# Performance work log

Measured on AMD Instinct MI355X. Metric: run time of the kernel, lower is better.

The kernel has to match this reference:

```python
import jax, jax.numpy as jnp
import numpy as np

DIM = 128      # size_in
SIGN = 4       # number of leading outputs negated
CONST = 0.618  # additive constant in Linear_v5
BATCH = 4096


def setup_inputs() -> dict:
    key = jax.random.key(0)
    k0, k1, k2, k3, k4 = jax.random.split(key, 5)
    s1 = 1.0 / np.sqrt(DIM)
    s2 = 1.0 / np.sqrt(2 * DIM)
    return {
        "t": 0,
        "input_": jax.random.normal(k0, (BATCH, 2 * DIM), dtype=jnp.float32),
        "W1": jax.random.uniform(k1, (2 * DIM, DIM), jnp.float32, -s1, s1),
        "b1": jax.random.uniform(k2, (2 * DIM,), jnp.float32, -s1, s1),
        "W2": jax.random.uniform(k3, (DIM, 2 * DIM), jnp.float32, -s2, s2),
        "b2": jax.random.uniform(k4, (DIM,), jnp.float32, -s2, s2),
    }


def reference(t, input_, W1, b1, W2, b2):
    x = input_[:, :DIM]   # [B, D]
    v = input_[:, DIM:]   # [B, D]
    dtype = x.dtype
    # sign vector: first SIGN outputs of g are negated (applied after sigmoid+const)
    sgn = jnp.where(jnp.arange(DIM) < SIGN, -1.0, 1.0).astype(dtype)  # [D]

    h = x @ W1.T + b1                      # [B, 2D]
    a = jax.nn.relu(h)
    s = jax.nn.sigmoid(a @ W2.T + b2)      # [B, D]
    g = sgn * (s + CONST)                  # [B, D]

    # Analytic batch Jacobian J[b,i,j] = d g_i / d x_j
    # = sgn_i * s_i(1-s_i) * sum_k W2[i,k] * 1[h_bk>0] * W1[k,j]
    mask = (h > 0).astype(dtype)           # [B, 2D]
    Jcore = jnp.einsum('ik,bk,kj->bij', W2, mask, W1)   # [B, D, D]
    J = (sgn * (s * (1.0 - s)))[:, :, None] * Jcore      # [B, D, D]

    g_inv = 1.0 / g                        # [B, D]
    conn1 = -J * g_inv[:, None, :]         # [B, i, j] * g_inv_j
    conn2 = J * g_inv[:, :, None]          # [B, i, j] * g_inv_i

    dv_vec = v[:, :, None] * v[:, None, :]               # [B, i, j] = v_i v_j
    vtemp1 = jnp.sum((v * v)[:, :, None] * conn1, axis=1)  # sum_i v_i^2 conn1[b,i,j]
    vtemp2 = jnp.einsum('bji,bji->bj', dv_vec, conn2)
    vtemp3 = jnp.einsum('bij,bji->bj', dv_vec, conn2)
    dv = vtemp1 + vtemp2 + vtemp3          # [B, D]

    return jnp.concatenate([v, dv], axis=1)  # [B, 2D]
```

## Files before the change

kernel.cpp:

```cpp
#include <hip/hip_runtime.h>
#include <math.h>

#define DIM    128
#define DIM2   256
#define NSIGN  4
#define CCONST 0.618f
#define MB     16
#define NTHR   512

typedef short bf16x8 __attribute__((ext_vector_type(8)));
typedef float f32x4  __attribute__((ext_vector_type(4)));

#define MFMA(a,b,c) __builtin_amdgcn_mfma_f32_16x16x32_bf16((a),(b),(c),0,0,0)

union BU { uint4 q; bf16x8 b; };

__device__ __forceinline__ unsigned short f2bf(float f) {
    unsigned u = __float_as_uint(f);
    u += 0x7fffu + ((u >> 16) & 1u);
    return (unsigned short)(u >> 16);
}
__device__ __forceinline__ float bf2f(unsigned short h) {
    return __uint_as_float(((unsigned)h) << 16);
}
__device__ __forceinline__ bf16x8 frag16(const unsigned short* p) {
    BU u; u.q = *(const uint4*)p; return u.b;
}

__global__ void prep_pack(const float* __restrict__ W1, const float* __restrict__ W2,
                          unsigned short* __restrict__ pk) {
    int tid  = blockIdx.x * 256 + threadIdx.x;
    int lane = tid & 63;
    int rest = tid >> 6;
    int es   = rest & 3;
    int tkt  = (rest >> 2) & 63;
    int m    = rest >> 8;
    int r0   = ((tkt & ((m == 0 || m == 2) ? 3 : 7)) * 32) + ((lane >> 4) << 3) + es * 2;
    int nt   = tkt / ((m == 0 || m == 2) ? 4 : 8);
    int c    = nt * 16 + (lane & 15);

    unsigned short h[2], l[2];
    #pragma unroll
    for (int d = 0; d < 2; ++d) {
        int r = r0 + d;
        float v;
        if      (m == 0) v = W1[c * DIM  + r];
        else if (m == 1) v = W2[c * DIM2 + r];
        else if (m == 2) v = W2[r * DIM2 + c];
        else             v = W1[r * DIM  + c];
        unsigned short hb = f2bf(v);
        h[d] = hb;
        if (m == 0) l[d] = f2bf(v - bf2f(hb));
    }
    size_t base = (size_t)m * 65536 + (size_t)(tkt * 64 + lane) * 8 + es * 2;
    *(unsigned*)(pk + base) = (unsigned)h[0] | ((unsigned)h[1] << 16);
    if (m == 0)
        *(unsigned*)(pk + base + 32768) = (unsigned)l[0] | ((unsigned)l[1] << 16);
}

__global__ __launch_bounds__(NTHR, 1)
void fused_connection(const float* __restrict__ input_,
                      const float* __restrict__ b1,
                      const float* __restrict__ b2,
                      const unsigned short* __restrict__ pk,
                      float* __restrict__ out) {
    __shared__ __align__(16) float          vv [MB][132];
    __shared__ __align__(16) unsigned short xbH[MB][136];
    __shared__ __align__(16) unsigned short xbL[MB][136];
    __shared__ __align__(16) unsigned short vbH[MB][136];
    __shared__ __align__(16) unsigned short aH [MB][264];
    __shared__ __align__(16) unsigned short mwH[MB][264];
    __shared__ __align__(16) unsigned short vcH[MB][136];

    const int t    = threadIdx.x;
    const int lane = t & 63;
    const int w    = t >> 6;
    const int b0   = blockIdx.x * MB;
    const int arow = lane & 15;
    const int kg   = (lane >> 4) << 3;
    const int rbase = (lane >> 4) << 2;

    const int prow = t >> 5;
    const int pc   = (t & 31) * 8;
    const float4* src = (const float4*)(input_ + (size_t)(b0 + prow) * DIM2 + pc);
    const float4 f0 = src[0];
    const float4 f1 = src[1];

    uint4 b1hq[2][4], b1lq[2][4];
    #pragma unroll
    for (int nt2 = 0; nt2 < 2; ++nt2)
        #pragma unroll
        for (int kt = 0; kt < 4; ++kt) {
            const unsigned short* bp = pk + (size_t)((((w * 2 + nt2) * 4 + kt) * 64 + lane) * 8);
            b1hq[nt2][kt] = *(const uint4*)bp;
            b1lq[nt2][kt] = *(const uint4*)(bp + 32768);
        }
    const float b1v0 = b1[(w * 2 + 0) * 16 + arow];
    const float b1v1 = b1[(w * 2 + 1) * 16 + arow];
    const float b2v  = b2[w * 16 + arow];

    {
        float fa[8] = {f0.x, f0.y, f0.z, f0.w, f1.x, f1.y, f1.z, f1.w};
        if (pc < DIM) {
            union { unsigned short u[8]; uint4 q; } H, L;
            #pragma unroll
            for (int e = 0; e < 8; ++e) {
                unsigned short hb = f2bf(fa[e]);
                H.u[e] = hb;
                L.u[e] = f2bf(fa[e] - bf2f(hb));
            }
            *(uint4*)&xbH[prow][pc] = H.q;
            *(uint4*)&xbL[prow][pc] = L.q;
        } else {
            int c = pc - DIM;
            *(float4*)&vv[prow][c]     = f0;
            *(float4*)&vv[prow][c + 4] = f1;
            union { unsigned short u[8]; uint4 q; } H;
            #pragma unroll
            for (int e = 0; e < 8; ++e) H.u[e] = f2bf(fa[e]);
            *(uint4*)&vbH[prow][c] = H.q;
            float4* op = (float4*)(out + (size_t)(b0 + prow) * DIM2 + c);
            op[0] = f0; op[1] = f1;
        }
    }
    __syncthreads();

    uint4 b2q[8];
    {
        const unsigned short* p1 = pk + 65536;
        #pragma unroll
        for (int kt = 0; kt < 8; ++kt)
            b2q[kt] = *(const uint4*)(p1 + (size_t)((w * 8 + kt) * 64 + lane) * 8);

        bf16x8 xH[4], xL[4], vH[4];
        #pragma unroll
        for (int kt = 0; kt < 4; ++kt) {
            int k0 = kt * 32 + kg;
            xH[kt] = frag16(&xbH[arow][k0]);
            xL[kt] = frag16(&xbL[arow][k0]);
            vH[kt] = frag16(&vbH[arow][k0]);
        }
        #pragma unroll
        for (int nt2 = 0; nt2 < 2; ++nt2) {
            int nt = w * 2 + nt2;
            f32x4 ha = {0.f, 0.f, 0.f, 0.f};
            f32x4 wa = {0.f, 0.f, 0.f, 0.f};
            #pragma unroll
            for (int kt = 0; kt < 4; ++kt) {
                BU bh, bl;
                bh.q = b1hq[nt2][kt];
                bl.q = b1lq[nt2][kt];
                ha = MFMA(xH[kt], bh.b, ha);
                ha = MFMA(xH[kt], bl.b, ha);
                ha = MFMA(xL[kt], bh.b, ha);
                wa = MFMA(vH[kt], bh.b, wa);
            }
            int col  = nt * 16 + arow;
            float bias = nt2 ? b1v1 : b1v0;
            #pragma unroll
            for (int reg = 0; reg < 4; ++reg) {
                int row = rbase + reg;
                float hv = ha[reg] + bias;
                bool  mk = hv > 0.f;
                aH[row][col]  = f2bf(mk ? hv : 0.f);
                mwH[row][col] = f2bf(mk ? wa[reg] : 0.f);
            }
        }
    }
    __syncthreads();

    float sreg[4];
    f32x4 t2a = {0.f, 0.f, 0.f, 0.f};
    uint4 b3q[2][4];
    {
        const unsigned short* p2 = pk + 2 * 65536;
        #pragma unroll
        for (int nt2 = 0; nt2 < 2; ++nt2)
            #pragma unroll
            for (int kt = 0; kt < 4; ++kt)
                b3q[nt2][kt] = *(const uint4*)(p2 + (size_t)((((w * 2 + nt2) * 4 + kt) * 64 + lane) * 8));

        f32x4 za = {0.f, 0.f, 0.f, 0.f};
        #pragma unroll
        for (int kt = 0; kt < 8; ++kt) {
            int k0 = kt * 32 + kg;
            bf16x8 af = frag16(&aH[arow][k0]);
            bf16x8 mf = frag16(&mwH[arow][k0]);
            BU bh; bh.q = b2q[kt];
            za  = MFMA(af, bh.b, za);
            t2a = MFMA(mf, bh.b, t2a);
        }
        int   ci   = w * 16 + arow;
        float sg_i = (ci < NSIGN) ? -1.f : 1.f;
        #pragma unroll
        for (int reg = 0; reg < 4; ++reg) {
            int row = rbase + reg;
            float z = za[reg] + b2v;
            float s = 1.f / (1.f + __expf(-z));
            sreg[reg] = s;
            float vvl = vv[row][ci];
            vcH[row][ci] = f2bf(vvl * vvl * sg_i * s * (1.f - s));
        }
    }
    __syncthreads();

    uint4 b4q[8];
    {
        const unsigned short* p3 = pk + 3 * 65536;
        #pragma unroll
        for (int kt = 0; kt < 8; ++kt)
            b4q[kt] = *(const uint4*)(p3 + (size_t)((w * 8 + kt) * 64 + lane) * 8);

        bf16x8 cH[4];
        #pragma unroll
        for (int kt = 0; kt < 4; ++kt)
            cH[kt] = frag16(&vcH[arow][kt * 32 + kg]);
        #pragma unroll
        for (int nt2 = 0; nt2 < 2; ++nt2) {
            int nt = w * 2 + nt2;
            f32x4 ua = {0.f, 0.f, 0.f, 0.f};
            #pragma unroll
            for (int kt = 0; kt < 4; ++kt) {
                BU bh; bh.q = b3q[nt2][kt];
                ua = MFMA(cH[kt], bh.b, ua);
            }
            int ck = nt * 16 + arow;
            #pragma unroll
            for (int reg = 0; reg < 4; ++reg) {
                int row = rbase + reg;
                bool mk = aH[row][ck] != 0;
                mwH[row][ck] = f2bf(mk ? ua[reg] : 0.f);
            }
        }
    }
    __syncthreads();

    {
        f32x4 t1a = {0.f, 0.f, 0.f, 0.f};
        #pragma unroll
        for (int kt = 0; kt < 8; ++kt) {
            bf16x8 mf = frag16(&mwH[arow][kt * 32 + kg]);
            BU bh; bh.q = b4q[kt];
            t1a = MFMA(mf, bh.b, t1a);
        }
        int   cj   = w * 16 + arow;
        float sg_j = (cj < NSIGN) ? -1.f : 1.f;
        #pragma unroll
        for (int reg = 0; reg < 4; ++reg) {
            int row = rbase + reg;
            float s  = sreg[reg];
            float cv = sg_j * s * (1.f - s);
            float gi = 1.f / (sg_j * (s + CCONST));
            float vvl = vv[row][cj];
            float dv = fmaf(-gi, t1a[reg], 2.f * vvl * gi * cv * t2a[reg]);
            out[(size_t)(b0 + row) * DIM2 + DIM + cj] = dv;
        }
    }
}

extern "C" void kernel_launch(void* const* d_in, const int* in_sizes, int n_in,
                              void* d_out, int out_size, void* d_ws, size_t ws_size,
                              hipStream_t stream) {
    const float* input_ = (const float*)d_in[1];
    const float* W1 = (const float*)d_in[2];
    const float* b1 = (const float*)d_in[3];
    const float* W2 = (const float*)d_in[4];
    const float* b2 = (const float*)d_in[5];
    float* out = (float*)d_out;
    unsigned short* pk = (unsigned short*)d_ws;

    const int batch = in_sizes[1] / DIM2;

    prep_pack<<<256, 256, 0, stream>>>(W1, W2, pk);
    fused_connection<<<batch / MB, NTHR, 0, stream>>>(input_, b1, b2, pk, out);
}
```

Measured before the change: 16.72 us.

## Run each 16-row tile with a single wavefront, replacing barriers with lgkmcnt waits

The block shrinks from eight waves to one. That single wave computes every column tile of all four GEMM stages itself, looping over pairs of N-tiles and loading the packed weights per pair. Because only one wave touches the LDS, the __syncthreads barriers become s_waitcnt lgkmcnt(0), which removes block-level synchronisation. The cost is eight times more serial MFMA work and weight traffic per wave. The launch presumably still uses 256 blocks of one wave each, far fewer waves than the 2048 before, so latency hiding and CU utilisation may suffer.

```diff
diff --git a/kernel.cpp b/kernel.cpp
--- a/kernel.cpp
+++ b/kernel.cpp
@@ -6,14 +6,15 @@
 #define NSIGN  4
 #define CCONST 0.618f
 #define MB     16
-#define NTHR   512
+#define NTHR   64
 
 typedef short bf16x8 __attribute__((ext_vector_type(8)));
 typedef float f32x4  __attribute__((ext_vector_type(4)));
 
 #define MFMA(a,b,c) __builtin_amdgcn_mfma_f32_16x16x32_bf16((a),(b),(c),0,0,0)
-
-union BU { uint4 q; bf16x8 b; };
+#define LGKM0() asm volatile("s_waitcnt lgkmcnt(0)" ::: "memory")
+
+union BU { uint4 q; bf16x8 b; unsigned short u[8]; };
 
 __device__ __forceinline__ unsigned short f2bf(float f) {
     unsigned u = __float_as_uint(f);
@@ -72,188 +73,232 @@
     __shared__ __align__(16) unsigned short mwH[MB][264];
     __shared__ __align__(16) unsigned short vcH[MB][136];
 
-    const int t    = threadIdx.x;
-    const int lane = t & 63;
-    const int w    = t >> 6;
-    const int b0   = blockIdx.x * MB;
-    const int arow = lane & 15;
-    const int kg   = (lane >> 4) << 3;
+    const int lane  = threadIdx.x;
+    const int b0    = blockIdx.x * MB;
+    const int arow  = lane & 15;
+    const int kg    = (lane >> 4) << 3;
     const int rbase = (lane >> 4) << 2;
 
-    const int prow = t >> 5;
-    const int pc   = (t & 31) * 8;
-    const float4* src = (const float4*)(input_ + (size_t)(b0 + prow) * DIM2 + pc);
-    const float4 f0 = src[0];
-    const float4 f1 = src[1];
-
-    uint4 b1hq[2][4], b1lq[2][4];
+    float4 fr[16];
     #pragma unroll
-    for (int nt2 = 0; nt2 < 2; ++nt2)
-        #pragma unroll
-        for (int kt = 0; kt < 4; ++kt) {
-            const unsigned short* bp = pk + (size_t)((((w * 2 + nt2) * 4 + kt) * 64 + lane) * 8);
-            b1hq[nt2][kt] = *(const uint4*)bp;
-            b1lq[nt2][kt] = *(const uint4*)(bp + 32768);
-        }
-    const float b1v0 = b1[(w * 2 + 0) * 16 + arow];
-    const float b1v1 = b1[(w * 2 + 1) * 16 + arow];
-    const float b2v  = b2[w * 16 + arow];
-
-    {
-        float fa[8] = {f0.x, f0.y, f0.z, f0.w, f1.x, f1.y, f1.z, f1.w};
-        if (pc < DIM) {
-            union { unsigned short u[8]; uint4 q; } H, L;
-            #pragma unroll
-            for (int e = 0; e < 8; ++e) {
+    for (int r = 0; r < 16; ++r)
+        fr[r] = *(const float4*)(input_ + (size_t)(b0 + r) * DIM2 + lane * 4);
+
+    if (lane < 32) {
+        const int c = lane * 4;
+        #pragma unroll
+        for (int r = 0; r < 16; ++r) {
+            float fa[4] = {fr[r].x, fr[r].y, fr[r].z, fr[r].w};
+            union { unsigned short u[4]; ushort4 q; } H, L;
+            #pragma unroll
+            for (int e = 0; e < 4; ++e) {
                 unsigned short hb = f2bf(fa[e]);
                 H.u[e] = hb;
                 L.u[e] = f2bf(fa[e] - bf2f(hb));
             }
-            *(uint4*)&xbH[prow][pc] = H.q;
-            *(uint4*)&xbL[prow][pc] = L.q;
-        } else {
-            int c = pc - DIM;
-            *(float4*)&vv[prow][c]     = f0;
-            *(float4*)&vv[prow][c + 4] = f1;
-            union { unsigned short u[8]; uint4 q; } H;
-            #pragma unroll
-            for (int e = 0; e < 8; ++e) H.u[e] = f2bf(fa[e]);
-            *(uint4*)&vbH[prow][c] = H.q;
-            float4* op = (float4*)(out + (size_t)(b0 + prow) * DIM2 + c);
-            op[0] = f0; op[1] = f1;
-        }
-    }
-    __syncthreads();
-
-    uint4 b2q[8];
+            *(ushort4*)&xbH[r][c] = H.q;
+            *(ushort4*)&xbL[r][c] = L.q;
+        }
+    } else {
+        const int c = lane * 4 - DIM;
+        #pragma unroll
+        for (int r = 0; r < 16; ++r) {
+            *(float4*)&vv[r][c] = fr[r];
+            float fa[4] = {fr[r].x, fr[r].y, fr[r].z, fr[r].w};
+            union { unsigned short u[4]; ushort4 q; } H;
+            #pragma unroll
+            for (int e = 0; e < 4; ++e) H.u[e] = f2bf(fa[e]);
+            *(ushort4*)&vbH[r][c] = H.q;
+            *(float4*)(out + (size_t)(b0 + r) * DIM2 + c) = fr[r];
+        }
+    }
+    LGKM0();
+
     {
-        const unsigned short* p1 = pk + 65536;
-        #pragma unroll
-        for (int kt = 0; kt < 8; ++kt)
-            b2q[kt] = *(const uint4*)(p1 + (size_t)((w * 8 + kt) * 64 + lane) * 8);
-
         bf16x8 xH[4], xL[4], vH[4];
         #pragma unroll
         for (int kt = 0; kt < 4; ++kt) {
-            int k0 = kt * 32 + kg;
+            const int k0 = kt * 32 + kg;
             xH[kt] = frag16(&xbH[arow][k0]);
             xL[kt] = frag16(&xbL[arow][k0]);
             vH[kt] = frag16(&vbH[arow][k0]);
         }
         #pragma unroll
-        for (int nt2 = 0; nt2 < 2; ++nt2) {
-            int nt = w * 2 + nt2;
-            f32x4 ha = {0.f, 0.f, 0.f, 0.f};
-            f32x4 wa = {0.f, 0.f, 0.f, 0.f};
+        for (int np = 0; np < 8; ++np) {
+            uint4 bh[2][4], bl[2][4];
+            #pragma unroll
+            for (int j = 0; j < 2; ++j)
+                #pragma unroll
+                for (int kt = 0; kt < 4; ++kt) {
+                    const unsigned short* bp =
+                        pk + (size_t)((((np * 2 + j) * 4 + kt) * 64 + lane) * 8);
+                    bh[j][kt] = *(const uint4*)bp;
+                    bl[j][kt] = *(const uint4*)(bp + 32768);
+                }
+            const float bv0 = b1[(np * 2 + 0) * 16 + arow];
+            const float bv1 = b1[(np * 2 + 1) * 16 + arow];
+            f32x4 ha0 = {0.f,0.f,0.f,0.f}, ha1 = {0.f,0.f,0.f,0.f};
+            f32x4 wa0 = {0.f,0.f,0.f,0.f}, wa1 = {0.f,0.f,0.f,0.f};
             #pragma unroll
             for (int kt = 0; kt < 4; ++kt) {
-                BU bh, bl;
-                bh.q = b1hq[nt2][kt];
-                bl.q = b1lq[nt2][kt];
-                ha = MFMA(xH[kt], bh.b, ha);
-                ha = MFMA(xH[kt], bl.b, ha);
-                ha = MFMA(xL[kt], bh.b, ha);
-                wa = MFMA(vH[kt], bh.b, wa);
-            }
-            int col  = nt * 16 + arow;
-            float bias = nt2 ? b1v1 : b1v0;
-            #pragma unroll
-            for (int reg = 0; reg < 4; ++reg) {
-                int row = rbase + reg;
-                float hv = ha[reg] + bias;
-                bool  mk = hv > 0.f;
-                aH[row][col]  = f2bf(mk ? hv : 0.f);
-                mwH[row][col] = f2bf(mk ? wa[reg] : 0.f);
-            }
-        }
-    }
-    __syncthreads();
-
-    float sreg[4];
-    f32x4 t2a = {0.f, 0.f, 0.f, 0.f};
-    uint4 b3q[2][4];
+                BU h0, l0, h1, l1;
+                h0.q = bh[0][kt]; l0.q = bl[0][kt];
+                h1.q = bh[1][kt]; l1.q = bl[1][kt];
+                ha0 = MFMA(xH[kt], h0.b, ha0);
+                ha1 = MFMA(xH[kt], h1.b, ha1);
+                ha0 = MFMA(xH[kt], l0.b, ha0);
+                ha1 = MFMA(xH[kt], l1.b, ha1);
+                ha0 = MFMA(xL[kt], h0.b, ha0);
+                ha1 = MFMA(xL[kt], h1.b, ha1);
+                wa0 = MFMA(vH[kt], h0.b, wa0);
+                wa1 = MFMA(vH[kt], h1.b, wa1);
+            }
+            #pragma unroll
+            for (int j = 0; j < 2; ++j) {
+                const int   col  = (np * 2 + j) * 16 + arow;
+                const float bias = j ? bv1 : bv0;
+                const f32x4 ha   = j ? ha1 : ha0;
+                const f32x4 wa   = j ? wa1 : wa0;
+                #pragma unroll
+                for (int reg = 0; reg < 4; ++reg) {
+                    const int row = rbase + reg;
+                    float hv = ha[reg] + bias;
+                    bool  mk = hv > 0.f;
+                    aH[row][col]  = f2bf(mk ? hv : 0.f);
+                    mwH[row][col] = f2bf(mk ? wa[reg] : 0.f);
+                }
+            }
+        }
+    }
+    LGKM0();
+
+    float sreg[8][4];
+    f32x4 t2s[8];
     {
-        const unsigned short* p2 = pk + 2 * 65536;
-        #pragma unroll
-        for (int nt2 = 0; nt2 < 2; ++nt2)
-            #pragma unroll
-            for (int kt = 0; kt < 4; ++kt)
-                b3q[nt2][kt] = *(const uint4*)(p2 + (size_t)((((w * 2 + nt2) * 4 + kt) * 64 + lane) * 8));
-
-        f32x4 za = {0.f, 0.f, 0.f, 0.f};
+        bf16x8 af[8], mf[8];
         #pragma unroll
         for (int kt = 0; kt < 8; ++kt) {
-            int k0 = kt * 32 + kg;
-            bf16x8 af = frag16(&aH[arow][k0]);
-            bf16x8 mf = frag16(&mwH[arow][k0]);
-            BU bh; bh.q = b2q[kt];
-            za  = MFMA(af, bh.b, za);
-            t2a = MFMA(mf, bh.b, t2a);
-        }
-        int   ci   = w * 16 + arow;
-        float sg_i = (ci < NSIGN) ? -1.f : 1.f;
-        #pragma unroll
-        for (int reg = 0; reg < 4; ++reg) {
-            int row = rbase + reg;
-            float z = za[reg] + b2v;
-            float s = 1.f / (1.f + __expf(-z));
-            sreg[reg] = s;
-            float vvl = vv[row][ci];
-            vcH[row][ci] = f2bf(vvl * vvl * sg_i * s * (1.f - s));
-        }
-    }
-    __syncthreads();
-
-    uint4 b4q[8];
+            const int k0 = kt * 32 + kg;
+            af[kt] = frag16(&aH[arow][k0]);
+            mf[kt] = frag16(&mwH[arow][k0]);
+        }
+        #pragma unroll
+        for (int cp = 0; cp < 4; ++cp) {
+            uint4 bq[2][8];
+            #pragma unroll
+            for (int j = 0; j < 2; ++j)
+                #pragma unroll
+                for (int kt = 0; kt < 8; ++kt)
+                    bq[j][kt] = *(const uint4*)(pk + 65536 +
+                        (size_t)((((cp * 2 + j) * 8 + kt) * 64 + lane) * 8));
+            const float b2v0 = b2[(cp * 2 + 0) * 16 + arow];
+            const float b2v1 = b2[(cp * 2 + 1) * 16 + arow];
+            f32x4 za0 = {0.f,0.f,0.f,0.f}, za1 = {0.f,0.f,0.f,0.f};
+            f32x4 t20 = {0.f,0.f,0.f,0.f}, t21 = {0.f,0.f,0.f,0.f};
+            #pragma unroll
+            for (int kt = 0; kt < 8; ++kt) {
+                BU q0, q1; q0.q = bq[0][kt]; q1.q = bq[1][kt];
+                za0 = MFMA(af[kt], q0.b, za0);
+                za1 = MFMA(af[kt], q1.b, za1);
+                t20 = MFMA(mf[kt], q0.b, t20);
+                t21 = MFMA(mf[kt], q1.b, t21);
+            }
+            #pragma unroll
+            for (int j = 0; j < 2; ++j) {
+                const int   ti = cp * 2 + j;
+                const int   ci = ti * 16 + arow;
+                const float sg = (ci < NSIGN) ? -1.f : 1.f;
+                const float bb = j ? b2v1 : b2v0;
+                const f32x4 za = j ? za1 : za0;
+                t2s[ti] = j ? t21 : t20;
+                #pragma unroll
+                for (int reg = 0; reg < 4; ++reg) {
+                    const int row = rbase + reg;
+                    float z = za[reg] + bb;
+                    float s = 1.f / (1.f + __expf(-z));
+                    sreg[ti][reg] = s;
+                    float vvl = vv[row][ci];
+                    vcH[row][ci] = f2bf(vvl * vvl * sg * s * (1.f - s));
+                }
+            }
+        }
+    }
+    LGKM0();
+
     {
-        const unsigned short* p3 = pk + 3 * 65536;
-        #pragma unroll
-        for (int kt = 0; kt < 8; ++kt)
-            b4q[kt] = *(const uint4*)(p3 + (size_t)((w * 8 + kt) * 64 + lane) * 8);
-
         bf16x8 cH[4];
         #pragma unroll
         for (int kt = 0; kt < 4; ++kt)
             cH[kt] = frag16(&vcH[arow][kt * 32 + kg]);
         #pragma unroll
-        for (int nt2 = 0; nt2 < 2; ++nt2) {
-            int nt = w * 2 + nt2;
-            f32x4 ua = {0.f, 0.f, 0.f, 0.f};
+        for (int np = 0; np < 8; ++np) {
+            uint4 bq[2][4];
+            #pragma unroll
+            for (int j = 0; j < 2; ++j)
+                #pragma unroll
+                for (int kt = 0; kt < 4; ++kt)
+                    bq[j][kt] = *(const uint4*)(pk + 2 * 65536 +
+                        (size_t)((((np * 2 + j) * 4 + kt) * 64 + lane) * 8));
+            f32x4 ua0 = {0.f,0.f,0.f,0.f}, ua1 = {0.f,0.f,0.f,0.f};
             #pragma unroll
             for (int kt = 0; kt < 4; ++kt) {
-                BU bh; bh.q = b3q[nt2][kt];
-                ua = MFMA(cH[kt], bh.b, ua);
-            }
-            int ck = nt * 16 + arow;
-            #pragma unroll
-            for (int reg = 0; reg < 4; ++reg) {
-                int row = rbase + reg;
-                bool mk = aH[row][ck] != 0;
-                mwH[row][ck] = f2bf(mk ? ua[reg] : 0.f);
-            }
-        }
-    }
-    __syncthreads();
+                BU q0, q1; q0.q = bq[0][kt]; q1.q = bq[1][kt];
+                ua0 = MFMA(cH[kt], q0.b, ua0);
+                ua1 = MFMA(cH[kt], q1.b, ua1);
+            }
+            #pragma unroll
+            for (int j = 0; j < 2; ++j) {
+                const int   ck = (np * 2 + j) * 16 + arow;
+                const f32x4 ua = j ? ua1 : ua0;
+                #pragma unroll
+                for (int reg = 0; reg < 4; ++reg) {
+                    const int row = rbase + reg;
+                    bool mk = aH[row][ck] != 0;
+                    mwH[row][ck] = f2bf(mk ? ua[reg] : 0.f);
+                }
+            }
+        }
+    }
+    LGKM0();
 
     {
-        f32x4 t1a = {0.f, 0.f, 0.f, 0.f};
-        #pragma unroll
-        for (int kt = 0; kt < 8; ++kt) {
-            bf16x8 mf = frag16(&mwH[arow][kt * 32 + kg]);
-            BU bh; bh.q = b4q[kt];
-            t1a = MFMA(mf, bh.b, t1a);
-        }
-        int   cj   = w * 16 + arow;
-        float sg_j = (cj < NSIGN) ? -1.f : 1.f;
-        #pragma unroll
-        for (int reg = 0; reg < 4; ++reg) {
-            int row = rbase + reg;
-            float s  = sreg[reg];
-            float cv = sg_j * s * (1.f - s);
-            float gi = 1.f / (sg_j * (s + CCONST));
-            float vvl = vv[row][cj];
-            float dv = fmaf(-gi, t1a[reg], 2.f * vvl * gi * cv * t2a[reg]);
-            out[(size_t)(b0 + row) * DIM2 + DIM + cj] = dv;
+        bf16x8 mu[8];
+        #pragma unroll
+        for (int kt = 0; kt < 8; ++kt)
+            mu[kt] = frag16(&mwH[arow][kt * 32 + kg]);
+        #pragma unroll
+        for (int cp = 0; cp < 4; ++cp) {
+            uint4 bq[2][8];
+            #pragma unroll
+            for (int j = 0; j < 2; ++j)
+                #pragma unroll
+                for (int kt = 0; kt < 8; ++kt)
+                    bq[j][kt] = *(const uint4*)(pk + 3 * 65536 +
+                        (size_t)((((cp * 2 + j) * 8 + kt) * 64 + lane) * 8));
+            f32x4 t10 = {0.f,0.f,0.f,0.f}, t11 = {0.f,0.f,0.f,0.f};
+            #pragma unroll
+            for (int kt = 0; kt < 8; ++kt) {
+                BU q0, q1; q0.q = bq[0][kt]; q1.q = bq[1][kt];
+                t10 = MFMA(mu[kt], q0.b, t10);
+                t11 = MFMA(mu[kt], q1.b, t11);
+            }
+            #pragma unroll
+            for (int j = 0; j < 2; ++j) {
+                const int   ti = cp * 2 + j;
+                const int   cj = ti * 16 + arow;
+                const float sg = (cj < NSIGN) ? -1.f : 1.f;
+                const f32x4 t1 = j ? t11 : t10;
+                #pragma unroll
+                for (int reg = 0; reg < 4; ++reg) {
+                    const int row = rbase + reg;
+                    float s  = sreg[ti][reg];
+                    float cv = sg * s * (1.f - s);
+                    float gi = 1.f / (sg * (s + CCONST));
+                    float vvl = vv[row][cj];
+                    float dv = fmaf(-gi, t1[reg], 2.f * vvl * gi * cv * t2s[ti][reg]);
+                    out[(size_t)(b0 + row) * DIM2 + DIM + cj] = dv;
+                }
+            }
         }
     }
 }
```

Result: slower. 28.87 us (+72.7%).
